# Kernel tuning notes

Measured on AMD Instinct MI355X. Metric: run time of the kernel, lower is better.

The kernel has to match this reference:

```python
import jax, jax.numpy as jnp
from jax import lax
import numpy as np

B, T, D, H, DH, FF, K = 16, 1024, 512, 8, 64, 2048, 3
EPS = 1e-5


def _layer_norm(x, g, b):
    mu = jnp.mean(x, axis=-1, keepdims=True)
    var = jnp.mean((x - mu) ** 2, axis=-1, keepdims=True)
    return (x - mu) / jnp.sqrt(var + EPS) * g + b


def setup_inputs() -> dict:
    key = jax.random.key(0)
    ks = jax.random.split(key, 14)
    f32 = jnp.float32
    dec_inp = jax.random.normal(ks[0], (B, T, D), f32)
    lengths = jax.random.randint(ks[1], (B,), T // 2, T + 1)
    mask = (jnp.arange(T)[None, :] < lengths[:, None])[:, :, None]  # [B,T,1] bool
    qkv_w = jax.random.normal(ks[2], (3 * H * DH, D), f32) * (D ** -0.5)
    qkv_b = jnp.zeros((3 * H * DH,), f32)
    o_w = jax.random.normal(ks[3], (D, H * DH), f32) * ((H * DH) ** -0.5)
    ln1_g = jnp.ones((D,), f32)
    ln1_b = jnp.zeros((D,), f32)
    conv1_w = jax.random.normal(ks[4], (FF, D, K), f32) * ((D * K) ** -0.5)
    conv1_b = jnp.zeros((FF,), f32)
    conv2_w = jax.random.normal(ks[5], (D, FF, K), f32) * ((FF * K) ** -0.5)
    conv2_b = jnp.zeros((D,), f32)
    ln2_g = jnp.ones((D,), f32)
    ln2_b = jnp.zeros((D,), f32)
    return dict(dec_inp=dec_inp, mask=mask, qkv_w=qkv_w, qkv_b=qkv_b, o_w=o_w,
                ln1_g=ln1_g, ln1_b=ln1_b, conv1_w=conv1_w, conv1_b=conv1_b,
                conv2_w=conv2_w, conv2_b=conv2_b, ln2_g=ln2_g, ln2_b=ln2_b)


def reference(dec_inp, mask, qkv_w, qkv_b, o_w, ln1_g, ln1_b,
              conv1_w, conv1_b, conv2_w, conv2_b, ln2_g, ln2_b):
    # ----- MultiHeadAttn (post-norm, dropout = identity in eval) -----
    attn_mask = ~mask[:, :, 0]                      # [B,T], True = pad
    qkv = dec_inp @ qkv_w.T + qkv_b                 # [B,T,3*H*DH]
    q, k, v = jnp.split(qkv, 3, axis=2)

    def to_heads(x):  # [B,T,H*DH] -> [B*H,T,DH] (batch-major, as in torch)
        return x.reshape(B, T, H, DH).transpose(0, 2, 1, 3).reshape(B * H, T, DH)

    q, k, v = to_heads(q), to_heads(k), to_heads(v)
    scores = jnp.einsum('bqd,bkd->bqk', q, k) * (DH ** -0.5)  # [B*H,T,T]
    # faithful to torch: mask tiled head-major (index i % B)
    am = jnp.tile(attn_mask[:, None, :], (H, T, 1))           # [B*H,T,T]
    scores = jnp.where(am, -jnp.inf, scores)
    prob = jax.nn.softmax(scores, axis=2)
    vec = jnp.einsum('bqk,bkd->bqd', prob, v)                 # [B*H,T,DH]
    # faithful to torch: view as [H,B,...] then permute
    vec = vec.reshape(H, B, T, DH).transpose(1, 2, 0, 3).reshape(B, T, H * DH)
    attn_out = vec @ o_w.T                                    # [B,T,D]
    out = _layer_norm(dec_inp + attn_out, ln1_g, ln1_b)
    out = out * mask

    # ----- PositionwiseConvFF (post-norm) -----
    x = out.transpose(0, 2, 1)                                # [B,D,T]
    h = lax.conv_general_dilated(x, conv1_w, (1,), [(K // 2, K // 2)],
                                 dimension_numbers=('NCH', 'OIH', 'NCH'))
    h = jax.nn.relu(h + conv1_b[None, :, None])
    h = lax.conv_general_dilated(h, conv2_w, (1,), [(K // 2, K // 2)],
                                 dimension_numbers=('NCH', 'OIH', 'NCH'))
    core = (h + conv2_b[None, :, None]).transpose(0, 2, 1)    # [B,T,D]
    out = _layer_norm(out + core, ln2_g, ln2_b)
    return out * mask
```

## Files before the change

kernel.cpp:

```cpp
#include <hip/hip_runtime.h>

using h16 = _Float16;
using h16x4 = __attribute__((ext_vector_type(4))) _Float16;
using h16x8 = __attribute__((ext_vector_type(8))) _Float16;
using f32x4 = __attribute__((ext_vector_type(4))) float;

static constexpr int cB = 16, cT = 1024, cD = 512, cH = 8, cDH = 64, cFF = 2048;
static constexpr int cM = cB * cT;
static constexpr int cTP = cT + 2;

__device__ __forceinline__ bool mask_val(const void* mb, int idx) {
  const unsigned char* u8 = (const unsigned char*)mb;
  if (u8[1] == 1) return u8[idx] != 0;
  const float* f = (const float*)mb;
  if (f[1] == 1.0f) return f[idx] != 0.0f;
  return ((const int*)mb)[idx] != 0;
}

__device__ __forceinline__ void gl_lds16(const h16* g, h16* l) {
  __builtin_amdgcn_global_load_lds(
      (const __attribute__((address_space(1))) unsigned int*)g,
      (__attribute__((address_space(3))) unsigned int*)l, 16, 0, 0);
}


__global__ __launch_bounds__(256) void k_cast4(const float* __restrict__ in,
                                               h16* __restrict__ out, int n4) {
  int i = blockIdx.x * 256 + threadIdx.x;
  if (i >= n4) return;
  const float4 f = ((const float4*)in)[i];
  h16x4 o = {(h16)f.x, (h16)f.y, (h16)f.z, (h16)f.w};
  ((h16x4*)out)[i] = o;
}

__global__ __launch_bounds__(256) void k_repack_w1(const float* __restrict__ w,
                                                   h16* __restrict__ out) {
  int i = blockIdx.x * 256 + threadIdx.x;
  if (i >= cFF * cD) return;
  int f = i >> 9, d = i & 511;
#pragma unroll
  for (int k = 0; k < 3; ++k)
    out[f * (3 * cD) + k * cD + d] = (h16)w[(long)i * 3 + k];
}

__global__ __launch_bounds__(256) void k_repack_w2(const float* __restrict__ w,
                                                   h16* __restrict__ out) {
  int i = blockIdx.x * 256 + threadIdx.x;
  if (i >= cD * cFF) return;
  int o = i >> 11, f = i & 2047;
#pragma unroll
  for (int k = 0; k < 3; ++k)
    out[o * (3 * cFF) + k * cFF + f] = (h16)w[(long)i * 3 + k];
}

__global__ __launch_bounds__(256) void k_zero_pads(h16* __restrict__ xp,
                                                   h16* __restrict__ hp) {
  int i = blockIdx.x * 256 + threadIdx.x;
  if (i < cB * 2 * cD) {
    int b = i / (2 * cD); int rr = (i / cD) & 1; int c = i % cD;
    xp[((long)b * cTP + rr * (cTP - 1)) * cD + c] = (h16)0.f;
  }
  if (i < cB * 2 * cFF) {
    int b = i / (2 * cFF); int rr = (i / cFF) & 1; int c = i % cFF;
    hp[((long)b * cTP + rr * (cTP - 1)) * cFF + c] = (h16)0.f;
  }
}

template <int SKIP, bool A_CONV, bool OUT_CONV, bool BIAS, bool RELU,
          bool OUT_H16, bool VSCAT, int SPLITK, bool SWIZ>
__global__ __launch_bounds__(256)
void gemm_bt(const h16* __restrict__ A, const h16* __restrict__ W,
             const float* __restrict__ bias, void* __restrict__ Cv,
             h16* __restrict__ Vg, const void* __restrict__ maskbuf,
             int ldc, int Kd, int lda, long zstride) {
  __shared__ h16 smem[2 * 128 * 64];
  h16* As = smem;
  h16* Bs = smem + 128 * 64;
  const int tid = threadIdx.x;
  const int w = tid >> 6, l = tid & 63;
  int m0, n0;
  if (SWIZ) {
    m0 = (blockIdx.x * 16 + (blockIdx.y >> 2)) * 128;
    n0 = (blockIdx.y & 3) * 128;
  } else {
    m0 = blockIdx.y * 128;
    n0 = blockIdx.x * 128;
  }

  if (SKIP == 1) {
    if (!mask_val(maskbuf, m0)) return;
  } else if (SKIP == 2) {
    int t0 = m0 & 1023, base = ((m0 >> 10) & 1) * 8;
    bool need = false;
#pragma unroll
    for (int i = 0; i < 8; ++i) need |= mask_val(maskbuf, ((base + i) << 10) + t0);
    if (!need) return;
  } else if (SKIP == 3) {
    int t0 = m0 & 1023;
    if (t0 && !mask_val(maskbuf, m0 - 1)) return;
  }

  const int wm = (w >> 1) * 64, wn = (w & 1) * 64;
  const int lr = l >> 3;
  const int lcs = ((l & 7) ^ lr) * 8;
  const int fr = l & 15;
  const int fb = fr & 7;
  const int qd = l >> 4;

  const int kspan = (SPLITK == 2) ? (Kd >> 1) : Kd;
  const int kbeg = (SPLITK == 2) ? blockIdx.z * kspan : 0;
  const int kend = kbeg + kspan;

  f32x4 zero4 = {0.f, 0.f, 0.f, 0.f};
  f32x4 acc[4][4];
#pragma unroll
  for (int mi = 0; mi < 4; ++mi)
#pragma unroll
    for (int ni = 0; ni < 4; ++ni) acc[mi][ni] = zero4;

  for (int k0 = kbeg; k0 < kend; k0 += 64) {
    __syncthreads();
#pragma unroll
    for (int i = 0; i < 4; ++i) {
      int c = w * 4 + i;
      int ar = m0 + c * 8 + lr;
      long aoff = (long)(ar + (A_CONV ? 2 * (ar >> 10) : 0)) * lda + k0 + lcs;
      gl_lds16(A + aoff, &As[c * 512]);
      int br = n0 + c * 8 + lr;
      long boff = (long)br * Kd + k0 + lcs;
      gl_lds16(W + boff, &Bs[c * 512]);
    }
    __syncthreads();
#pragma unroll
    for (int kc = 0; kc < 2; ++kc) {
      h16x8 af[4], bfr[4];
#pragma unroll
      for (int mi = 0; mi < 4; ++mi)
        af[mi] = *(const h16x8*)&As[(wm + mi * 16 + fr) * 64 +
                                    (((kc * 4 + qd) ^ fb) * 8)];
#pragma unroll
      for (int ni = 0; ni < 4; ++ni)
        bfr[ni] = *(const h16x8*)&Bs[(wn + ni * 16 + fr) * 64 +
                                     (((kc * 4 + qd) ^ fb) * 8)];
#pragma unroll
      for (int mi = 0; mi < 4; ++mi)
#pragma unroll
        for (int ni = 0; ni < 4; ++ni)
          acc[mi][ni] = __builtin_amdgcn_mfma_f32_16x16x32_f16(
              af[mi], bfr[ni], acc[mi][ni], 0, 0, 0);
    }
  }
  const bool do_bias = BIAS && (SPLITK == 1 || blockIdx.z == 0);
  if (VSCAT && n0 >= 1024) {
#pragma unroll
    for (int mi = 0; mi < 4; ++mi) {
      int t0 = (m0 + wm + mi * 16 + (l >> 4) * 4) & 1023;
      int jj = ((m0 >> 10) << 3);
#pragma unroll
      for (int ni = 0; ni < 4; ++ni) {
        int gc = n0 + wn + ni * 16 + fr;
        int dh = gc & 63;
        int j2 = jj + ((gc - 1024) >> 6);
        float bb = do_bias ? bias[gc] : 0.f;
        h16x4 v4 = {(h16)(acc[mi][ni][0] + bb), (h16)(acc[mi][ni][1] + bb),
                    (h16)(acc[mi][ni][2] + bb), (h16)(acc[mi][ni][3] + bb)};
        *(h16x4*)&Vg[((long)j2 * 64 + dh) * 1024 + t0] = v4;
      }
    }
  } else if (OUT_H16) {
    __syncthreads();
#pragma unroll
    for (int mi = 0; mi < 4; ++mi) {
#pragma unroll
      for (int ni = 0; ni < 4; ++ni) {
#pragma unroll
        for (int rr = 0; rr < 4; ++rr) {
          int rrow = wm + mi * 16 + (l >> 4) * 4 + rr;
          int ccol = wn + ni * 16 + fr;
          float v = acc[mi][ni][rr];
          if (do_bias) v += bias[n0 + ccol];
          if (RELU) v = v > 0.f ? v : 0.f;
          smem[rrow * 128 + ccol] = (h16)v;
        }
      }
    }
    __syncthreads();
    h16* outp = (h16*)Cv + (SPLITK == 2 ? (long)blockIdx.z * zstride : 0);
    const int r2 = tid >> 4, c2 = (tid & 15) * 8;
#pragma unroll
    for (int i = 0; i < 8; ++i) {
      int row = r2 + i * 16;
      int gr = m0 + row;
      long orow = (long)gr + (OUT_CONV ? (2 * (gr >> 10) + 1) : 0);
      *(h16x8*)&outp[orow * ldc + n0 + c2] = *(h16x8*)&smem[row * 128 + c2];
    }
  } else {
#pragma unroll
    for (int mi = 0; mi < 4; ++mi) {
#pragma unroll
      for (int ni = 0; ni < 4; ++ni) {
#pragma unroll
        for (int rr = 0; rr < 4; ++rr) {
          int gr = m0 + wm + mi * 16 + (l >> 4) * 4 + rr;
          int gc = n0 + wn + ni * 16 + fr;
          float v = acc[mi][ni][rr];
          if (do_bias) v += bias[gc];
          if (RELU) v = v > 0.f ? v : 0.f;
          long orow = (long)gr + (OUT_CONV ? (2 * (gr >> 10) + 1) : 0);
          ((float*)Cv)[orow * ldc + gc] = v;
        }
      }
    }
  }
}

__global__ __launch_bounds__(256)
void k_attn(const h16* __restrict__ qk, const h16* __restrict__ Vg,
            const void* __restrict__ maskbuf, h16* __restrict__ attn_out) {
  __shared__ h16 Ks[64 * 64];
  __shared__ h16 Vt[64 * 64];
  __shared__ h16 Ps[4][16 * 68];
  __shared__ float sbias[64];
  const int tid = threadIdx.x, w = tid >> 6, l = tid & 63;
  const int f = blockIdx.x;
  const int bp = f & 15, qt = (f >> 4) & 15, hp = f >> 8;
  const int j = hp * 16 + bp;
  const int bd = j >> 3, hd = j & 7;

  if (!mask_val(maskbuf, bp * cT + qt * 64)) return;

  const int fr = l & 15, fq = (l >> 4) * 8;
  const int fb = fr & 7, qd = l >> 4;
  const int lr = l >> 3, lcs = ((l & 7) ^ lr) * 8;

  h16x8 qf[2];
#pragma unroll
  for (int kc = 0; kc < 2; ++kc) {
    qf[kc] = *(const h16x8*)&qk[
        (long)((bd << 10) + qt * 64 + w * 16 + fr) * 1024 +
        hd * 64 + kc * 32 + fq];
    qf[kc] *= (h16)0.125f;
  }

  f32x4 zero4 = {0.f, 0.f, 0.f, 0.f};
  f32x4 o[4];
  float lrow[4];
#pragma unroll
  for (int nt = 0; nt < 4; ++nt) o[nt] = zero4;
#pragma unroll
  for (int r = 0; r < 4; ++r) lrow[r] = 0.f;

  for (int k0 = 0; k0 < cT; k0 += 64) {
    if (!mask_val(maskbuf, bp * cT + k0)) break;
    __syncthreads();
#pragma unroll
    for (int i = 0; i < 2; ++i) {
      int c = w * 2 + i;
      int row = c * 8 + lr;
      gl_lds16(qk + (long)((bd << 10) + k0 + row) * 1024 + 512 + hd * 64 + lcs,
               &Ks[c * 512]);
      gl_lds16(Vg + ((long)j * 64 + row) * 1024 + k0 + lcs, &Vt[c * 512]);
    }
    if (tid < 64)
      sbias[tid] = mask_val(maskbuf, bp * cT + k0 + tid) ? 0.f : -1e30f;
    __syncthreads();

    f32x4 S[4];
#pragma unroll
    for (int kt = 0; kt < 4; ++kt) {
      float sb = sbias[kt * 16 + fr];
      f32x4 s = {sb, sb, sb, sb};
#pragma unroll
      for (int kc = 0; kc < 2; ++kc) {
        h16x8 kf = *(const h16x8*)&Ks[(kt * 16 + fr) * 64 +
                                      (((kc * 4 + qd) ^ fb) * 8)];
        s = __builtin_amdgcn_mfma_f32_16x16x32_f16(qf[kc], kf, s, 0, 0, 0);
      }
      S[kt] = s;
    }
#pragma unroll
    for (int r = 0; r < 4; ++r) {
      float p0 = __expf(S[0][r] - 4.f), p1 = __expf(S[1][r] - 4.f);
      float p2 = __expf(S[2][r] - 4.f), p3 = __expf(S[3][r] - 4.f);
      lrow[r] += (p0 + p1) + (p2 + p3);
      int ql = (l >> 4) * 4 + r;
      Ps[w][ql * 68 + fr] = (h16)p0;
      Ps[w][ql * 68 + 16 + fr] = (h16)p1;
      Ps[w][ql * 68 + 32 + fr] = (h16)p2;
      Ps[w][ql * 68 + 48 + fr] = (h16)p3;
    }
#pragma unroll
    for (int kp = 0; kp < 2; ++kp) {
      h16x8 pf = *(const h16x8*)&Ps[w][fr * 68 + kp * 32 + fq];
#pragma unroll
      for (int nt = 0; nt < 4; ++nt) {
        h16x8 vf = *(const h16x8*)&Vt[(nt * 16 + fr) * 64 +
                                      (((kp * 4 + qd) ^ fb) * 8)];
        o[nt] = __builtin_amdgcn_mfma_f32_16x16x32_f16(pf, vf, o[nt], 0, 0, 0);
      }
    }
  }
#pragma unroll
  for (int r = 0; r < 4; ++r) {
#pragma unroll
    for (int m = 1; m < 16; m <<= 1) lrow[r] += __shfl_xor(lrow[r], m);
    float inv = 1.f / lrow[r];
    int q = qt * 64 + w * 16 + (l >> 4) * 4 + r;
    long row = (long)bp * cT + q;
#pragma unroll
    for (int nt = 0; nt < 4; ++nt)
      attn_out[row * cD + hp * 64 + nt * 16 + fr] = (h16)(o[nt][r] * inv);
  }
}

template <bool WRITE_XP, bool RH16, bool R2H16>
__global__ __launch_bounds__(256)
void k_ln(const float* __restrict__ X, const void* __restrict__ Rv,
          const void* __restrict__ Rv2,
          const float* __restrict__ g, const float* __restrict__ bta,
          const void* __restrict__ maskbuf,
          float* __restrict__ outf, h16* __restrict__ xp) {
  const int w = threadIdx.x >> 6, l = threadIdx.x & 63;
  const long row = (long)blockIdx.x * 4 + w;
  const float4* x4 = (const float4*)(X + row * cD);
  float4 a0 = x4[l], a1 = x4[l + 64];
  float v[8];
  if (RH16) {
    const h16x4* r4 = (const h16x4*)((const h16*)Rv + row * cD);
    h16x4 b0 = r4[l], b1 = r4[l + 64];
    v[0] = a0.x + (float)b0[0]; v[1] = a0.y + (float)b0[1];
    v[2] = a0.z + (float)b0[2]; v[3] = a0.w + (float)b0[3];
    v[4] = a1.x + (float)b1[0]; v[5] = a1.y + (float)b1[1];
    v[6] = a1.z + (float)b1[2]; v[7] = a1.w + (float)b1[3];
  } else {
    const float4* r4 = (const float4*)((const float*)Rv + row * cD);
    float4 b0 = r4[l], b1 = r4[l + 64];
    v[0] = a0.x + b0.x; v[1] = a0.y + b0.y; v[2] = a0.z + b0.z; v[3] = a0.w + b0.w;
    v[4] = a1.x + b1.x; v[5] = a1.y + b1.y; v[6] = a1.z + b1.z; v[7] = a1.w + b1.w;
  }
  if (R2H16) {
    const h16x4* r4 = (const h16x4*)((const h16*)Rv2 + row * cD);
    h16x4 b0 = r4[l], b1 = r4[l + 64];
    v[0] += (float)b0[0]; v[1] += (float)b0[1];
    v[2] += (float)b0[2]; v[3] += (float)b0[3];
    v[4] += (float)b1[0]; v[5] += (float)b1[1];
    v[6] += (float)b1[2]; v[7] += (float)b1[3];
  }
  float s = 0.f;
#pragma unroll
  for (int i = 0; i < 8; ++i) s += v[i];
#pragma unroll
  for (int m = 1; m < 64; m <<= 1) s += __shfl_xor(s, m);
  const float mu = s * (1.f / 512.f);
  float s2 = 0.f;
#pragma unroll
  for (int i = 0; i < 8; ++i) { float d = v[i] - mu; s2 += d * d; }
#pragma unroll
  for (int m = 1; m < 64; m <<= 1) s2 += __shfl_xor(s2, m);
  const float rstd = rsqrtf(s2 * (1.f / 512.f) + 1e-5f);
  const float mv = mask_val(maskbuf, (int)row) ? 1.f : 0.f;
  const float4* g4 = (const float4*)g;
  const float4* t4 = (const float4*)bta;
  float4 g0 = g4[l], g1 = g4[l + 64], t0 = t4[l], t1 = t4[l + 64];
  float4 y0, y1;
  y0.x = ((v[0] - mu) * rstd * g0.x + t0.x) * mv;
  y0.y = ((v[1] - mu) * rstd * g0.y + t0.y) * mv;
  y0.z = ((v[2] - mu) * rstd * g0.z + t0.z) * mv;
  y0.w = ((v[3] - mu) * rstd * g0.w + t0.w) * mv;
  y1.x = ((v[4] - mu) * rstd * g1.x + t1.x) * mv;
  y1.y = ((v[5] - mu) * rstd * g1.y + t1.y) * mv;
  y1.z = ((v[6] - mu) * rstd * g1.z + t1.z) * mv;
  y1.w = ((v[7] - mu) * rstd * g1.w + t1.w) * mv;
  ((float4*)(outf + row * cD))[l] = y0;
  ((float4*)(outf + row * cD))[l + 64] = y1;
  if (WRITE_XP) {
    const long xrow = row + 2 * (row >> 10) + 1;
    h16x4 h0 = {(h16)y0.x, (h16)y0.y, (h16)y0.z, (h16)y0.w};
    h16x4 h1 = {(h16)y1.x, (h16)y1.y, (h16)y1.z, (h16)y1.w};
    ((h16x4*)(xp + xrow * cD))[l] = h0;
    ((h16x4*)(xp + xrow * cD))[l + 64] = h1;
  }
}

extern "C" void kernel_launch(void* const* d_in, const int* in_sizes, int n_in,
                              void* d_out, int out_size, void* d_ws, size_t ws_size,
                              hipStream_t stream) {
  const float* dec   = (const float*)d_in[0];
  const void*  maskb = d_in[1];
  const float* qkv_w = (const float*)d_in[2];
  const float* qkv_b = (const float*)d_in[3];
  const float* o_w   = (const float*)d_in[4];
  const float* ln1g  = (const float*)d_in[5];
  const float* ln1b  = (const float*)d_in[6];
  const float* c1w   = (const float*)d_in[7];
  const float* c1b   = (const float*)d_in[8];
  const float* c2w   = (const float*)d_in[9];
  const float* c2b   = (const float*)d_in[10];
  const float* ln2g  = (const float*)d_in[11];
  const float* ln2b  = (const float*)d_in[12];

  char* p = (char*)d_ws;
  auto alloc = [&](size_t bytes) {
    char* r = p; p += (bytes + 255) & ~(size_t)255; return r;
  };
  h16*   dec_h  = (h16*)alloc((size_t)cM * cD * 2);
  h16*   qkvw_h = (h16*)alloc((size_t)1536 * cD * 2);
  h16*   ow_h   = (h16*)alloc((size_t)cD * cD * 2);
  h16*   w1p    = (h16*)alloc((size_t)cFF * 3 * cD * 2);
  h16*   w2p    = (h16*)alloc((size_t)cD * 3 * cFF * 2);
  h16*   qk_h   = (h16*)alloc((size_t)cM * 1024 * 2);
  h16*   vg     = (h16*)alloc((size_t)cB * cH * cDH * cT * 2);
  h16*   attn_h = (h16*)alloc((size_t)cM * cD * 2);
  float* tmp    = (float*)alloc((size_t)cM * cD * 4);
  float* out1   = (float*)alloc((size_t)cM * cD * 4);
  h16*   xp     = (h16*)alloc((size_t)cB * cTP * cD * 2);
  h16*   hp     = (h16*)alloc((size_t)cB * cTP * cFF * 2);
  h16*   core0 = attn_h;
  h16*   core1 = qk_h;
  (void)ws_size; (void)n_in; (void)in_sizes; (void)out_size;

  k_cast4<<<(cM * cD / 4 + 255) / 256, 256, 0, stream>>>(dec, dec_h, cM * cD / 4);
  k_cast4<<<(1536 * cD / 4 + 255) / 256, 256, 0, stream>>>(qkv_w, qkvw_h, 1536 * cD / 4);
  k_cast4<<<(cD * cD / 4 + 255) / 256, 256, 0, stream>>>(o_w, ow_h, cD * cD / 4);
  k_repack_w1<<<(cFF * cD + 255) / 256, 256, 0, stream>>>(c1w, w1p);
  k_repack_w2<<<(cD * cFF + 255) / 256, 256, 0, stream>>>(c2w, w2p);
  k_zero_pads<<<(cB * 2 * cFF + 255) / 256, 256, 0, stream>>>(xp, hp);

  gemm_bt<2, false, false, true, false, true, true, 1, false>
      <<<dim3(12, cM / 128), 256, 0, stream>>>(dec_h, qkvw_h, qkv_b, qk_h, vg,
                                               maskb, 1024, cD, cD, 0);

  k_attn<<<dim3(2048), 256, 0, stream>>>(qk_h, vg, maskb, attn_h);

  gemm_bt<1, false, false, false, false, false, false, 1, false>
      <<<dim3(cD / 128, cM / 128), 256, 0, stream>>>(attn_h, ow_h, nullptr, tmp,
                                                     nullptr, maskb, cD, cD, cD, 0);

  k_ln<true, false, false><<<cM / 4, 256, 0, stream>>>(dec, tmp, nullptr, ln1g,
                                                       ln1b, maskb, out1, xp);

  gemm_bt<3, true, true, true, true, true, false, 1, false>
      <<<dim3(cFF / 128, cM / 128), 256, 0, stream>>>(xp, w1p, c1b, hp, nullptr,
                                                      maskb, cFF, 3 * cD, cD, 0);

  gemm_bt<1, true, false, true, false, true, false, 2, true>
      <<<dim3(8, 64, 2), 256, 0, stream>>>(hp, w2p, c2b, core0, nullptr,
                                           maskb, cD, 3 * cFF, cFF,
                                           (long)(core1 - core0));

  k_ln<false, true, true><<<cM / 4, 256, 0, stream>>>(out1, core0, core1, ln2g,
                                                      ln2b, maskb,
                                                      (float*)d_out, nullptr);
}
```

Before: 552.3 us.

## Add 256x256-tile 512-thread GEMM kernel for the two conv FFN layers

Adds a new GEMM kernel with 256x256 output tiles, 8 waves, a double-buffered 128KB dynamic-LDS pipeline using direct global-to-LDS loads, and an LDS-staged vectorized fp16 epilogue. It replaces the previous 128x128 GEMMs for both conv1 (with ReLU and padded output) and conv2 (split-K by 2), keeping the existing mask-based tile skipping. The larger tile is meant to raise arithmetic intensity and cut global traffic per FLOP. In exchange there are fewer blocks, coarser mask skipping granularity, and heavy register and LDS pressure, which limits occupancy.

Measured after the change: 501.5 us. -9.2%, faster.

```diff
diff --git a/kernel.cpp b/kernel.cpp
--- a/kernel.cpp
+++ b/kernel.cpp
@@ -211,6 +211,141 @@
         }
       }
     }
+  }
+}
+
+template <int SKIP, bool A_CONV, bool OUT_CONV, bool BIAS, bool RELU,
+          int SPLITK, int NBLK_LOG2>
+__global__ __launch_bounds__(512, 2)
+void gemm8(const h16* __restrict__ A, const h16* __restrict__ W,
+           const float* __restrict__ bias, h16* __restrict__ C,
+           const void* __restrict__ maskbuf, int ldc, int Kd, int lda,
+           long zstride) {
+  extern __shared__ h16 sm[];
+  const int tid = threadIdx.x;
+  const int wid = tid >> 6, l = tid & 63;
+  const int m0 = (blockIdx.x * 8 + (blockIdx.y >> NBLK_LOG2)) * 256;
+  const int n0 = (blockIdx.y & ((1 << NBLK_LOG2) - 1)) * 256;
+
+  if (SKIP == 1) {
+    if (!mask_val(maskbuf, m0)) return;
+  } else if (SKIP == 3) {
+    int t0 = m0 & 1023;
+    if (t0 && !mask_val(maskbuf, m0 - 1)) return;
+  }
+
+  const int wm = wid >> 2, wn = wid & 3;
+  const int fr = l & 15, qd = l >> 4, fb = fr & 7;
+  const int lr = l >> 3;
+  const int lcs = ((l & 7) ^ lr) * 8;
+
+  const int kspan = (SPLITK == 2) ? (Kd >> 1) : Kd;
+  const int kbeg = (SPLITK == 2) ? blockIdx.z * kspan : 0;
+  const int nt = kspan >> 6;
+
+  f32x4 zero4 = {0.f, 0.f, 0.f, 0.f};
+  f32x4 acc[8][4];
+#pragma unroll
+  for (int m = 0; m < 8; ++m)
+#pragma unroll
+    for (int n = 0; n < 4; ++n) acc[m][n] = zero4;
+
+  auto stage = [&](int ti, h16* Ab, h16* Bb) {
+#pragma unroll
+    for (int i = 0; i < 4; ++i) {
+      int c = wid * 4 + i;
+      int ar = m0 + c * 8 + lr;
+      long aoff = (long)(ar + (A_CONV ? 2 * (ar >> 10) : 0)) * lda +
+                  kbeg + ti * 64 + lcs;
+      gl_lds16(A + aoff, &Ab[c * 512]);
+      int br = n0 + c * 8 + lr;
+      long boff = (long)br * Kd + kbeg + ti * 64 + lcs;
+      gl_lds16(W + boff, &Bb[c * 512]);
+    }
+  };
+
+  stage(0, sm, sm + 16384);
+  stage(1, sm + 32768, sm + 49152);
+  asm volatile("s_waitcnt vmcnt(8)" ::: "memory");
+  __builtin_amdgcn_s_barrier();
+
+  const int arow = wm * 128 + fr;
+  const int brow = wn * 64 + fr;
+  const int sA = (qd ^ fb) * 8;
+  const int sB = ((4 + qd) ^ fb) * 8;
+
+  for (int t = 0; t < nt; ++t) {
+    h16* Ab = sm + (t & 1) * 32768;
+    h16* Bb = Ab + 16384;
+    h16x8 a0[8], b0[4];
+#pragma unroll
+    for (int m = 0; m < 8; ++m)
+      a0[m] = *(const h16x8*)&Ab[(arow + m * 16) * 64 + sA];
+#pragma unroll
+    for (int n = 0; n < 4; ++n)
+      b0[n] = *(const h16x8*)&Bb[(brow + n * 16) * 64 + sA];
+    __builtin_amdgcn_s_setprio(1);
+#pragma unroll
+    for (int m = 0; m < 8; ++m)
+#pragma unroll
+      for (int n = 0; n < 4; ++n)
+        acc[m][n] = __builtin_amdgcn_mfma_f32_16x16x32_f16(a0[m], b0[n],
+                                                           acc[m][n], 0, 0, 0);
+    __builtin_amdgcn_s_setprio(0);
+    h16x8 a1[8], b1[4];
+#pragma unroll
+    for (int m = 0; m < 8; ++m)
+      a1[m] = *(const h16x8*)&Ab[(arow + m * 16) * 64 + sB];
+#pragma unroll
+    for (int n = 0; n < 4; ++n)
+      b1[n] = *(const h16x8*)&Bb[(brow + n * 16) * 64 + sB];
+    asm volatile("s_waitcnt lgkmcnt(0)" ::: "memory");
+    __builtin_amdgcn_s_barrier();
+    const bool pf = (t + 2 < nt);
+    if (pf) stage(t + 2, Ab, Bb);
+    __builtin_amdgcn_s_setprio(1);
+#pragma unroll
+    for (int m = 0; m < 8; ++m)
+#pragma unroll
+      for (int n = 0; n < 4; ++n)
+        acc[m][n] = __builtin_amdgcn_mfma_f32_16x16x32_f16(a1[m], b1[n],
+                                                           acc[m][n], 0, 0, 0);
+    __builtin_amdgcn_s_setprio(0);
+    if (t + 1 < nt) {
+      if (pf)
+        asm volatile("s_waitcnt vmcnt(8)" ::: "memory");
+      else
+        asm volatile("s_waitcnt vmcnt(0)" ::: "memory");
+      __builtin_amdgcn_s_barrier();
+    }
+  }
+
+  const bool do_bias = BIAS && (SPLITK == 1 || blockIdx.z == 0);
+  const int qd4 = qd * 4;
+#pragma unroll
+  for (int m = 0; m < 8; ++m) {
+    int row = wm * 128 + m * 16 + qd4;
+#pragma unroll
+    for (int n = 0; n < 4; ++n) {
+      int col = wn * 64 + n * 16 + fr;
+      float bb = do_bias ? bias[n0 + col] : 0.f;
+#pragma unroll
+      for (int rr = 0; rr < 4; ++rr) {
+        float v = acc[m][n][rr] + bb;
+        if (RELU) v = v > 0.f ? v : 0.f;
+        sm[(row + rr) * 256 + col] = (h16)v;
+      }
+    }
+  }
+  __syncthreads();
+  h16* outp = C + (SPLITK == 2 ? (long)blockIdx.z * zstride : 0);
+  const int r2 = tid >> 5, c2 = (tid & 31) * 8;
+#pragma unroll
+  for (int i = 0; i < 16; ++i) {
+    int row = r2 + i * 16;
+    int gr = m0 + row;
+    long orow = (long)gr + (OUT_CONV ? (2 * (gr >> 10) + 1) : 0);
+    *(h16x8*)&outp[orow * (long)ldc + n0 + c2] = *(h16x8*)&sm[row * 256 + c2];
   }
 }
 
@@ -419,6 +554,17 @@
   h16*   core1 = qk_h;
   (void)ws_size; (void)n_in; (void)in_sizes; (void)out_size;
 
+  static bool s_attr = false;
+  if (!s_attr) {
+    hipFuncSetAttribute(
+        reinterpret_cast<const void*>(&gemm8<3, true, true, true, true, 1, 3>),
+        hipFuncAttributeMaxDynamicSharedMemorySize, 131072);
+    hipFuncSetAttribute(
+        reinterpret_cast<const void*>(&gemm8<1, true, false, true, false, 2, 1>),
+        hipFuncAttributeMaxDynamicSharedMemorySize, 131072);
+    s_attr = true;
+  }
+
   k_cast4<<<(cM * cD / 4 + 255) / 256, 256, 0, stream>>>(dec, dec_h, cM * cD / 4);
   k_cast4<<<(1536 * cD / 4 + 255) / 256, 256, 0, stream>>>(qkv_w, qkvw_h, 1536 * cD / 4);
   k_cast4<<<(cD * cD / 4 + 255) / 256, 256, 0, stream>>>(o_w, ow_h, cD * cD / 4);
@@ -439,14 +585,14 @@
   k_ln<true, false, false><<<cM / 4, 256, 0, stream>>>(dec, tmp, nullptr, ln1g,
                                                        ln1b, maskb, out1, xp);
 
-  gemm_bt<3, true, true, true, true, true, false, 1, false>
-      <<<dim3(cFF / 128, cM / 128), 256, 0, stream>>>(xp, w1p, c1b, hp, nullptr,
-                                                      maskb, cFF, 3 * cD, cD, 0);
-
-  gemm_bt<1, true, false, true, false, true, false, 2, true>
-      <<<dim3(8, 64, 2), 256, 0, stream>>>(hp, w2p, c2b, core0, nullptr,
-                                           maskb, cD, 3 * cFF, cFF,
-                                           (long)(core1 - core0));
+  gemm8<3, true, true, true, true, 1, 3>
+      <<<dim3(8, 64), dim3(512), 131072, stream>>>(xp, w1p, c1b, hp, maskb,
+                                                   cFF, 3 * cD, cD, 0);
+
+  gemm8<1, true, false, true, false, 2, 1>
+      <<<dim3(8, 16, 2), dim3(512), 131072, stream>>>(hp, w2p, c2b, core0,
+                                                      maskb, cD, 3 * cFF, cFF,
+                                                      (long)(core1 - core0));
 
   k_ln<false, true, true><<<cM / 4, 256, 0, stream>>>(out1, core0, core1, ln2g,
                                                       ln2b, maskb,
```
